# Kernel optimization log

Measured on AMD Instinct MI355X. Metric: run time of the kernel, lower is better.

Reference implementation:

```python
import jax, jax.numpy as jnp
import numpy as np

B, S, H = 1, 2048, 1024
NH, KVH, HD = 16, 4, 64
E, TOPK, F = 8, 2, 2048
EPS = 1e-5
THETA = 10000.0


def setup_inputs() -> dict:
    key = jax.random.key(0)
    ks = jax.random.split(key, 12)
    s = 0.02
    return {
        "hidden_states": jax.random.normal(ks[0], (B, S, H), jnp.float32),
        "position_ids": jnp.arange(S, dtype=jnp.int64).reshape(1, S),
        "ln1_w": jnp.ones((H,), jnp.float32),
        "ln2_w": jnp.ones((H,), jnp.float32),
        "wq": jax.random.normal(ks[1], (NH * HD, H), jnp.float32) * s,
        "wk": jax.random.normal(ks[2], (KVH * HD, H), jnp.float32) * s,
        "wv": jax.random.normal(ks[3], (KVH * HD, H), jnp.float32) * s,
        "wo": jax.random.normal(ks[4], (H, NH * HD), jnp.float32) * s,
        "gate_w": jax.random.normal(ks[5], (E, H), jnp.float32) * s,
        "w1": jax.random.normal(ks[6], (E, F, H), jnp.float32) * s,
        "w2": jax.random.normal(ks[7], (E, H, F), jnp.float32) * s,
        "w3": jax.random.normal(ks[8], (E, F, H), jnp.float32) * s,
    }


def rmsnorm(x, w, eps=EPS):
    xf = x.astype(jnp.float32)
    v = jnp.mean(xf * xf, axis=-1, keepdims=True)
    return (xf * jax.lax.rsqrt(v + eps)).astype(x.dtype) * w


def rotate_half(x):
    x1, x2 = jnp.split(x, 2, axis=-1)
    return jnp.concatenate([-x2, x1], axis=-1)


def attention(x, position_ids, wq, wk, wv, wo):
    q = (x @ wq.T).reshape(B, S, NH, HD).transpose(0, 2, 1, 3)   # [B,NH,S,HD]
    k = (x @ wk.T).reshape(B, S, KVH, HD).transpose(0, 2, 1, 3)  # [B,KVH,S,HD]
    v = (x @ wv.T).reshape(B, S, KVH, HD).transpose(0, 2, 1, 3)
    inv_freq = 1.0 / (THETA ** (jnp.arange(0, HD, 2, dtype=jnp.float32) / HD))
    ang = position_ids.astype(jnp.float32)[:, :, None] * inv_freq  # [B,S,HD/2]
    emb = jnp.concatenate([ang, ang], axis=-1)                     # [B,S,HD]
    cos = jnp.cos(emb)[:, None]                                    # [B,1,S,HD]
    sin = jnp.sin(emb)[:, None]
    q = q * cos + rotate_half(q) * sin
    k = k * cos + rotate_half(k) * sin
    rep = NH // KVH
    k = jnp.repeat(k, rep, axis=1)
    v = jnp.repeat(v, rep, axis=1)
    scores = jnp.einsum("bhqd,bhkd->bhqk", q, k) / np.sqrt(HD).astype(np.float32)
    causal = jnp.tril(jnp.ones((S, S), bool))
    scores = jnp.where(causal, scores, jnp.finfo(scores.dtype).min)
    attn = jax.nn.softmax(scores, axis=-1)
    ctx = jnp.einsum("bhqk,bhkd->bhqd", attn, v)
    ctx = ctx.transpose(0, 2, 1, 3).reshape(B, S, NH * HD)
    return ctx @ wo.T


def moe(x, gate_w, w1, w2, w3):
    xt = x.reshape(-1, H)                                  # [T,H]
    router_logits = xt @ gate_w.T                          # [T,E]
    probs = jax.nn.softmax(router_logits.astype(jnp.float32), axis=-1)
    topw, topi = jax.lax.top_k(probs, TOPK)                # [T,K]
    topw = topw / jnp.sum(topw, axis=-1, keepdims=True)
    topw = topw.astype(x.dtype)
    # combine weights per expert: [T,E]
    cw = jnp.sum(topw[..., None] * jax.nn.one_hot(topi, E, dtype=x.dtype), axis=1)
    h1 = jnp.einsum("th,efh->etf", xt, w1)
    h3 = jnp.einsum("th,efh->etf", xt, w3)
    g = jax.nn.silu(h1) * h3                               # [E,T,F]
    y = jnp.einsum("etf,ehf->eth", g, w2)                  # [E,T,H]
    out = jnp.einsum("eth,te->th", y, cw)
    return out.reshape(B, S, H), router_logits


def reference(hidden_states, position_ids, ln1_w, ln2_w, wq, wk, wv, wo,
              gate_w, w1, w2, w3):
    residual = hidden_states
    h = rmsnorm(hidden_states, ln1_w)
    h = attention(h, position_ids, wq, wk, wv, wo)
    h = residual + h
    residual = h
    h = rmsnorm(h, ln2_w)
    h, router_logits = moe(h, gate_w, w1, w2, w3)
    h = residual + h
    return h, router_logits
```

## Files before the change

### kernel.cpp

```cpp
#include <hip/hip_runtime.h>
#include <hip/hip_bf16.h>
#include <cstdint>

typedef unsigned short u16;
typedef __attribute__((ext_vector_type(8))) short bh8;
typedef __attribute__((ext_vector_type(4))) short sh4;
typedef __attribute__((ext_vector_type(4))) float fx4;

#define NTOK 2048
#define HDIM 1024
#define NE 8
#define FDIM 2048

__device__ __forceinline__ u16 f2bf(float f) {
    __hip_bfloat16 h = __float2bfloat16(f);
    return __builtin_bit_cast(u16, h);
}

__device__ __forceinline__ void gll16(const void* g, void* l) {
    __builtin_amdgcn_global_load_lds(
        (const __attribute__((address_space(1))) void*)g,
        (__attribute__((address_space(3))) void*)l, 16, 0, 0);
}

__global__ __launch_bounds__(256)
void convert_k(const float* __restrict__ S, u16* __restrict__ D, int n8) {
    int i = blockIdx.x * 256 + threadIdx.x;
    const int stride = gridDim.x * 256;
    for (; i < n8; i += stride) {
        const fx4 a = *(const fx4*)&S[(size_t)i * 8];
        const fx4 b = *(const fx4*)&S[(size_t)i * 8 + 4];
        bh8 o;
        #pragma unroll
        for (int j = 0; j < 4; ++j) {
            o[j]     = (short)f2bf(a[j]);
            o[j + 4] = (short)f2bf(b[j]);
        }
        *(bh8*)&D[(size_t)i * 8] = o;
    }
}

__global__ __launch_bounds__(256)
void rope_table_k(float* __restrict__ cosT, float* __restrict__ sinT) {
    int idx = blockIdx.x * 256 + threadIdx.x;
    int t = idx >> 5, i = idx & 31;
    float freq = powf(10000.0f, -(float)i * (1.0f / 32.0f));
    float ang = (float)t * freq;
    float s, c;
    sincosf(ang, &s, &c);
    cosT[idx] = c;
    sinT[idx] = s;
}

__global__ __launch_bounds__(256)
void rmsnorm_k(const float* __restrict__ X, const float* __restrict__ W, u16* __restrict__ O) {
    const int t = blockIdx.x;
    const int tid = threadIdx.x;
    const fx4 v = *(const fx4*)&X[(size_t)t * HDIM + tid * 4];
    float ss = v[0]*v[0] + v[1]*v[1] + v[2]*v[2] + v[3]*v[3];
    #pragma unroll
    for (int o = 1; o < 64; o <<= 1) ss += __shfl_xor(ss, o);
    __shared__ float red[4];
    if ((tid & 63) == 0) red[tid >> 6] = ss;
    __syncthreads();
    const float inv = rsqrtf((red[0] + red[1] + red[2] + red[3]) * (1.0f / HDIM) + 1e-5f);
// ... 22 lines not shown
    fx4 xn;
    #pragma unroll
    for (int i = 0; i < 4; ++i) xn[i] = v[i] * inv * w[i];
    sh4 o4;
    #pragma unroll
    for (int i = 0; i < 4; ++i) o4[i] = (short)f2bf(xn[i]);
    *(sh4*)&O[(size_t)t * HDIM + tid * 4] = o4;

    float part[NE];
    #pragma unroll
    for (int e = 0; e < NE; ++e) {
        const fx4 g = *(const fx4*)&GW[(size_t)e * HDIM + tid * 4];
        part[e] = g[0]*xn[0] + g[1]*xn[1] + g[2]*xn[2] + g[3]*xn[3];
    }
    #pragma unroll
    for (int e = 0; e < NE; ++e)
        #pragma unroll
        for (int o = 1; o < 64; o <<= 1) part[e] += __shfl_xor(part[e], o);
    __shared__ float red8[4][NE];
    if ((tid & 63) == 0) {
        #pragma unroll
        for (int e = 0; e < NE; ++e) red8[tid >> 6][e] = part[e];
    }
    __syncthreads();
    if (tid < NE)
        LOGI[(size_t)t * NE + tid] = red8[0][tid] + red8[1][tid] + red8[2][tid] + red8[3][tid];
}

__global__ __launch_bounds__(256)
void router_topk_k(const float* __restrict__ LOGI, int* __restrict__ counts,
                   int* __restrict__ tokslot, float* __restrict__ wtb) {
    const int t = blockIdx.x * 256 + threadIdx.x;
    float l[NE];
    #pragma unroll
    for (int e = 0; e < NE; ++e) l[e] = LOGI[(size_t)t * NE + e];
    int i0 = 0;
    #pragma unroll
    for (int e = 1; e < NE; ++e) if (l[e] > l[i0]) i0 = e;
    int i1 = (i0 == 0) ? 1 : 0;
    #pragma unroll
    for (int e = 0; e < NE; ++e) if (e != i0 && l[e] > l[i1]) i1 = e;
    float e1 = __expf(l[i1] - l[i0]);
    float w0 = 1.0f / (1.0f + e1);
    float w1 = 1.0f - w0;
    int p0 = atomicAdd(&counts[i0], 1);
    tokslot[i0 * NTOK + p0] = t * 2;
    wtb[i0 * NTOK + p0] = w0;
    int p1 = atomicAdd(&counts[i1], 1);
    tokslot[i1 * NTOK + p1] = t * 2 + 1;
    wtb[i1 * NTOK + p1] = w1;
}

template<int EPI>
__global__ __launch_bounds__(256)
void gemm_bt(const u16* __restrict__ A, const u16* __restrict__ B,
             u16* __restrict__ Cb, float* __restrict__ Cf,
             const int N, const int K,
             const float* __restrict__ aux0, const float* __restrict__ aux1) {
    __shared__ u16 As[2][64 * 32];
    __shared__ u16 Bs[2][64 * 32];

    const int tid = threadIdx.x;
    const int lane = tid & 63;
    const int wid = tid >> 6;
    const int lrow = lane & 15, lgrp = lane >> 4;
    const int wm = wid * 16;

    const int m0 = blockIdx.y * 64;
    const int n0 = blockIdx.x * 64;

    const u16* apg = A + (size_t)(m0 + (tid >> 2)) * K + (tid & 3) * 8;
    const u16* bpg = B + (size_t)(n0 + (tid >> 2)) * K + (tid & 3) * 8;

    fx4 acc[4];
    #pragma unroll
    for (int i = 0; i < 4; ++i) acc[i] = fx4{0.f, 0.f, 0.f, 0.f};

    gll16(apg, &As[0][wid * 512]);
    gll16(bpg, &Bs[0][wid * 512]);
    int cur = 0;
    for (int k0 = 0; k0 < K; k0 += 32) {
        __syncthreads();
        if (k0 + 32 < K) {
            gll16(apg + k0 + 32, &As[cur ^ 1][wid * 512]);
            gll16(bpg + k0 + 32, &Bs[cur ^ 1][wid * 512]);
        }
        const bh8 af = *(const bh8*)&As[cur][(wm + lrow) * 32 + lgrp * 8];
        #pragma unroll
        for (int ni = 0; ni < 4; ++ni) {
            const bh8 bf = *(const bh8*)&Bs[cur][(ni * 16 + lrow) * 32 + lgrp * 8];
            acc[ni] = __builtin_amdgcn_mfma_f32_16x16x32_bf16(af, bf, acc[ni], 0, 0, 0);
        }
        cur ^= 1;
    }

    #pragma unroll
    for (int j = 0; j < 4; ++j) {
        const int r = m0 + wm + lgrp * 4 + j;
        if (EPI == 3) {
            #pragma unroll
            for (int ni = 0; ni < 2; ++ni) {
                const int d = ni * 16 + lrow;
                const float cv = aux0[r * 32 + d];
                const float sv = aux1[r * 32 + d];
                const float v0 = acc[ni][j];
                const float v1 = acc[ni + 2][j];
                Cb[(size_t)r * N + n0 + d]      = f2bf(v0 * cv - v1 * sv);
                Cb[(size_t)r * N + n0 + d + 32] = f2bf(v1 * cv + v0 * sv);
            }
        } else {
            #pragma unroll
            for (int ni = 0; ni < 4; ++ni) {
                const int c = n0 + ni * 16 + lrow;
                const float v = acc[ni][j];
                if (EPI == 1) Cf[(size_t)r * N + c] = v + aux0[(size_t)r * N + c];
                if (EPI == 2) Cb[(size_t)r * N + c] = f2bf(v);
            }
        }
    }
}

__global__ __launch_bounds__(256)
void attn_kernel(const u16* __restrict__ Q, const u16* __restrict__ Kg,
                 const u16* __restrict__ Vg, u16* __restrict__ O) {
    const int qt = blockIdx.x;
    const int h = blockIdx.y;
    const int kvh = h >> 2;

    const int tid = threadIdx.x;
    const int lane = tid & 63;
    const int wid = tid >> 6;
    const int lrow = lane & 15, lgrp = lane >> 4;

    __shared__ u16 Ks[64 * 72];
    __shared__ u16 Vs[64 * 72];
    __shared__ u16 Ps[4][32 * 72];

    const int qbase = qt * 128 + wid * 32;

    bh8 qf[2][2];
    #pragma unroll
    for (int mi = 0; mi < 2; ++mi)
        #pragma unroll
        for (int kf = 0; kf < 2; ++kf)
            qf[mi][kf] = *(const bh8*)&Q[(size_t)(qbase + mi * 16 + lrow) * 1024 + h * 64 + kf * 32 + lgrp * 8];

    fx4 acc[2][4];
    #pragma unroll
    for (int mi = 0; mi < 2; ++mi)
        #pragma unroll
        for (int ni = 0; ni < 4; ++ni) acc[mi][ni] = fx4{0.f, 0.f, 0.f, 0.f};
    float mrun[2][4], lrun[2][4];
    #pragma unroll
    for (int mi = 0; mi < 2; ++mi)
        #pragma unroll
        for (int j = 0; j < 4; ++j) { mrun[mi][j] = -1e30f; lrun[mi][j] = 0.f; }

    const int srow = tid >> 2;
    const int sseg = (tid & 3) * 16;

    const int ntiles = qt * 2 + 2;

    size_t goff = (size_t)(srow) * 256 + kvh * 64 + sseg;
    bh8 kva = *(const bh8*)&Kg[goff];
    bh8 kvb = *(const bh8*)&Kg[goff + 8];
    bh8 vva = *(const bh8*)&Vg[goff];
    bh8 vvb = *(const bh8*)&Vg[goff + 8];

    for (int it = 0; it < ntiles; ++it) {
// ... 56 lines not shown
                const float alpha = __expf(mrun[mi][j] - mnew);
                mrun[mi][j] = mnew;
                float rsum = 0.f;
                #pragma unroll
                for (int nf = 0; nf < 4; ++nf) {
                    const float p = __expf(s[mi][nf][j] - mnew);
                    s[mi][nf][j] = p;
                    rsum += p;
                }
                #pragma unroll
                for (int o = 1; o < 16; o <<= 1) rsum += __shfl_xor(rsum, o);
                lrun[mi][j] = lrun[mi][j] * alpha + rsum;
                #pragma unroll
                for (int ni = 0; ni < 4; ++ni) acc[mi][ni][j] *= alpha;
            }

        u16* pw = Ps[wid];
        #pragma unroll
        for (int mi = 0; mi < 2; ++mi)
            #pragma unroll
            for (int nf = 0; nf < 4; ++nf)
                #pragma unroll
                for (int j = 0; j < 4; ++j)
                    pw[(mi * 16 + lgrp * 4 + j) * 72 + nf * 16 + lrow] = f2bf(s[mi][nf][j]);

        #pragma unroll
        for (int kf = 0; kf < 2; ++kf) {
            bh8 pa[2];
            #pragma unroll
            for (int mi = 0; mi < 2; ++mi)
                pa[mi] = *(const bh8*)&pw[(mi * 16 + lrow) * 72 + kf * 32 + lgrp * 8];
            #pragma unroll
            for (int ni = 0; ni < 4; ++ni) {
                bh8 vb = *(const bh8*)&Vs[(ni * 16 + lrow) * 72 + kf * 32 + lgrp * 8];
                #pragma unroll
                for (int mi = 0; mi < 2; ++mi)
                    acc[mi][ni] = __builtin_amdgcn_mfma_f32_16x16x32_bf16(pa[mi], vb, acc[mi][ni], 0, 0, 0);
            }
        }
    }

    #pragma unroll
    for (int mi = 0; mi < 2; ++mi)
        #pragma unroll
        for (int j = 0; j < 4; ++j) {
            const float inv = 1.0f / lrun[mi][j];
            const int r = qbase + mi * 16 + lgrp * 4 + j;
            #pragma unroll
            for (int ni = 0; ni < 4; ++ni)
                O[(size_t)r * 1024 + h * 64 + ni * 16 + lrow] = f2bf(acc[mi][ni][j] * inv);
        }
}

__global__ __launch_bounds__(256)
void moe_up_k(const u16* __restrict__ X, const u16* __restrict__ W1b,
              const u16* __restrict__ W3b, const int* __restrict__ counts,
              const int* __restrict__ tokslot, u16* __restrict__ G) {
    const int e = blockIdx.z;
    const int cnt = counts[e];
    const int m0 = blockIdx.y * 64;
    if (m0 >= cnt) return;
    const int n0 = blockIdx.x * 128;

    __shared__ u16 As[2][64 * 32];
    __shared__ u16 B1s[2][128 * 32];
    __shared__ u16 B3s[2][128 * 32];

    const int tid = threadIdx.x;
    const int lane = tid & 63, wid = tid >> 6;
    const int wm = (wid >> 1) * 32, wn = (wid & 1) * 64;
    const int lrow = lane & 15, lgrp = lane >> 4;

    const int p = m0 + (tid >> 2);
    const int tok = (p < cnt) ? (tokslot[e * NTOK + p] >> 1) : 0;
    const u16* apg  = X + (size_t)tok * HDIM + (tid & 3) * 8;
    const u16* b1pg = W1b + (size_t)e * FDIM * HDIM + (size_t)(n0 + (tid >> 2)) * HDIM + (tid & 3) * 8;
    const u16* b3pg = W3b + (size_t)e * FDIM * HDIM + (size_t)(n0 + (tid >> 2)) * HDIM + (tid & 3) * 8;

    fx4 acc1[2][4], acc3[2][4];
    #pragma unroll
    for (int i = 0; i < 2; ++i)
        #pragma unroll
        for (int j = 0; j < 4; ++j) {
            acc1[i][j] = fx4{0.f, 0.f, 0.f, 0.f};
            acc3[i][j] = fx4{0.f, 0.f, 0.f, 0.f};
        }

    gll16(apg, &As[0][wid * 512]);
    gll16(b1pg, &B1s[0][wid * 512]);
    gll16(b1pg + (size_t)64 * HDIM, &B1s[0][2048 + wid * 512]);
    gll16(b3pg, &B3s[0][wid * 512]);
    gll16(b3pg + (size_t)64 * HDIM, &B3s[0][2048 + wid * 512]);

    int cur = 0;
    for (int k0 = 0; k0 < HDIM; k0 += 32) {
        __syncthreads();
        if (k0 + 32 < HDIM) {
            const int kn = k0 + 32;
            gll16(apg + kn, &As[cur ^ 1][wid * 512]);
            gll16(b1pg + kn, &B1s[cur ^ 1][wid * 512]);
            gll16(b1pg + (size_t)64 * HDIM + kn, &B1s[cur ^ 1][2048 + wid * 512]);
            gll16(b3pg + kn, &B3s[cur ^ 1][wid * 512]);
            gll16(b3pg + (size_t)64 * HDIM + kn, &B3s[cur ^ 1][2048 + wid * 512]);
        }
        bh8 af[2];
        #pragma unroll
        for (int mi = 0; mi < 2; ++mi)
            af[mi] = *(const bh8*)&As[cur][(wm + mi * 16 + lrow) * 32 + lgrp * 8];
        #pragma unroll
        for (int ni = 0; ni < 4; ++ni) {
            const bh8 b1f = *(const bh8*)&B1s[cur][(wn + ni * 16 + lrow) * 32 + lgrp * 8];
            const bh8 b3f = *(const bh8*)&B3s[cur][(wn + ni * 16 + lrow) * 32 + lgrp * 8];
            #pragma unroll
            for (int mi = 0; mi < 2; ++mi) {
                acc1[mi][ni] = __builtin_amdgcn_mfma_f32_16x16x32_bf16(af[mi], b1f, acc1[mi][ni], 0, 0, 0);
                acc3[mi][ni] = __builtin_amdgcn_mfma_f32_16x16x32_bf16(af[mi], b3f, acc3[mi][ni], 0, 0, 0);
            }
        }
        cur ^= 1;
    }

    #pragma unroll
    for (int mi = 0; mi < 2; ++mi)
        #pragma unroll
        for (int j = 0; j < 4; ++j) {
            const int r = m0 + wm + mi * 16 + lgrp * 4 + j;
            if (r < cnt) {
                #pragma unroll
                for (int ni = 0; ni < 4; ++ni) {
                    const int c = n0 + wn + ni * 16 + lrow;
                    const float h1 = acc1[mi][ni][j];
                    const float h3 = acc3[mi][ni][j];
                    const float gv = h1 / (1.0f + __expf(-h1)) * h3;
                    G[((size_t)e * NTOK + r) * FDIM + c] = f2bf(gv);
                }
            }
        }
}

__global__ __launch_bounds__(256)
void moe_down_k(const u16* __restrict__ G, const u16* __restrict__ W2b,
                const int* __restrict__ counts, const int* __restrict__ tokslot,
                const float* __restrict__ wtb, float* __restrict__ MO) {
    const int e = blockIdx.z;
    const int cnt = counts[e];
    const int m0 = blockIdx.y * 64;
    if (m0 >= cnt) return;
    const int n0 = blockIdx.x * 64;

    __shared__ u16 As[2][64 * 32];
    __shared__ u16 Bs[2][64 * 32];

    const int tid = threadIdx.x;
    const int lane = tid & 63, wid = tid >> 6;
    const int wm = wid * 16;
    const int lrow = lane & 15, lgrp = lane >> 4;

    const u16* apg = G + ((size_t)e * NTOK + m0 + (tid >> 2)) * FDIM + (tid & 3) * 8;
    const u16* bpg = W2b + (size_t)e * HDIM * FDIM + (size_t)(n0 + (tid >> 2)) * FDIM + (tid & 3) * 8;

    fx4 acc[4];
    #pragma unroll
    for (int i = 0; i < 4; ++i) acc[i] = fx4{0.f, 0.f, 0.f, 0.f};

    gll16(apg, &As[0][wid * 512]);
    gll16(bpg, &Bs[0][wid * 512]);
    int cur = 0;
    for (int k0 = 0; k0 < FDIM; k0 += 32) {
        __syncthreads();
        if (k0 + 32 < FDIM) {
            gll16(apg + k0 + 32, &As[cur ^ 1][wid * 512]);
            gll16(bpg + k0 + 32, &Bs[cur ^ 1][wid * 512]);
        }
        const bh8 af = *(const bh8*)&As[cur][(wm + lrow) * 32 + lgrp * 8];
        #pragma unroll
        for (int ni = 0; ni < 4; ++ni) {
            const bh8 bf = *(const bh8*)&Bs[cur][(ni * 16 + lrow) * 32 + lgrp * 8];
            acc[ni] = __builtin_amdgcn_mfma_f32_16x16x32_bf16(af, bf, acc[ni], 0, 0, 0);
        }
        cur ^= 1;
    }

    #pragma unroll
    for (int j = 0; j < 4; ++j) {
        const int r = m0 + wm + lgrp * 4 + j;
        if (r < cnt) {
            const int ts = tokslot[e * NTOK + r];
            const float wgt = wtb[e * NTOK + r];
            const int tt = ts >> 1;
            const int sl = ts & 1;
            #pragma unroll
            for (int ni = 0; ni < 4; ++ni) {
                const int c = n0 + ni * 16 + lrow;
                MO[((size_t)sl * NTOK + tt) * HDIM + c] = acc[ni][j] * wgt;
            }
        }
    }
}

__global__ __launch_bounds__(256)
void final_add_k(const float* __restrict__ A, const float* __restrict__ B0,
                 const float* __restrict__ B1, float* __restrict__ O) {
    const size_t i = ((size_t)blockIdx.x * 256 + threadIdx.x) * 4;
    const fx4 a = *(const fx4*)&A[i];
    const fx4 b = *(const fx4*)&B0[i];
    const fx4 c = *(const fx4*)&B1[i];
    fx4 r;
    #pragma unroll
    for (int k = 0; k < 4; ++k) r[k] = a[k] + b[k] + c[k];
    *(fx4*)&O[i] = r;
}

extern "C" void kernel_launch(void* const* d_in, const int* in_sizes, int n_in,
                              void* d_out, int out_size, void* d_ws, size_t ws_size,
                              hipStream_t stream) {
    const float* x   = (const float*)d_in[0];
    const float* ln1 = (const float*)d_in[2];
    const float* ln2 = (const float*)d_in[3];
    const float* wq  = (const float*)d_in[4];
    const float* wk  = (const float*)d_in[5];
    const float* wv  = (const float*)d_in[6];
    const float* wo  = (const float*)d_in[7];
    const float* gw  = (const float*)d_in[8];
    const float* w1  = (const float*)d_in[9];
    const float* w2  = (const float*)d_in[10];
    const float* w3  = (const float*)d_in[11];

    float* out_h = (float*)d_out;
    float* out_logits = out_h + (size_t)NTOK * HDIM;

    uint8_t* wsb = (uint8_t*)d_ws;
    size_t off = 0;
    auto alloc = [&](size_t bytes) -> void* {
        void* ptr = wsb + off;
        off = (off + bytes + 255) & ~(size_t)255;
        return ptr;
    };
    u16*   xn1    = (u16*)alloc((size_t)NTOK * HDIM * 2);
    u16*   qb     = (u16*)alloc((size_t)NTOK * 1024 * 2);
    u16*   kb     = (u16*)alloc((size_t)NTOK * 256 * 2);
    u16*   vb     = (u16*)alloc((size_t)NTOK * 256 * 2);
    u16*   ctxb   = (u16*)alloc((size_t)NTOK * 1024 * 2);
    float* hattn  = (float*)alloc((size_t)NTOK * HDIM * 4);
    u16*   xn2    = (u16*)alloc((size_t)NTOK * HDIM * 2);
    float* cosT   = (float*)alloc((size_t)NTOK * 32 * 4);
    float* sinT   = (float*)alloc((size_t)NTOK * 32 * 4);
    int*   counts = (int*)alloc(NE * 4);
    int*   tokslot= (int*)alloc((size_t)NE * NTOK * 4);
    float* wtb    = (float*)alloc((size_t)NE * NTOK * 4);
    u16*   gbuf   = (u16*)alloc((size_t)NE * NTOK * FDIM * 2);
    float* moeb   = (float*)alloc((size_t)2 * NTOK * HDIM * 4);
    u16*   wqb    = (u16*)alloc((size_t)1024 * HDIM * 2);
    u16*   wkb    = (u16*)alloc((size_t)256 * HDIM * 2);
    u16*   wvb    = (u16*)alloc((size_t)256 * HDIM * 2);
    u16*   wob    = (u16*)alloc((size_t)HDIM * 1024 * 2);
    u16*   w1b    = (u16*)alloc((size_t)NE * FDIM * HDIM * 2);
    u16*   w2b    = (u16*)alloc((size_t)NE * HDIM * FDIM * 2);
    u16*   w3b    = (u16*)alloc((size_t)NE * FDIM * HDIM * 2);

    hipMemsetAsync(counts, 0, NE * 4, stream);

    convert_k<<<512, 256, 0, stream>>>(wq, wqb, 1024 * HDIM / 8);
    convert_k<<<128, 256, 0, stream>>>(wk, wkb, 256 * HDIM / 8);
    convert_k<<<128, 256, 0, stream>>>(wv, wvb, 256 * HDIM / 8);
    convert_k<<<512, 256, 0, stream>>>(wo, wob, HDIM * 1024 / 8);
    convert_k<<<2048, 256, 0, stream>>>(w1, w1b, NE * FDIM * HDIM / 8);
    convert_k<<<2048, 256, 0, stream>>>(w2, w2b, NE * HDIM * FDIM / 8);
    convert_k<<<2048, 256, 0, stream>>>(w3, w3b, NE * FDIM * HDIM / 8);

    rope_table_k<<<256, 256, 0, stream>>>(cosT, sinT);
    rmsnorm_k<<<NTOK, 256, 0, stream>>>(x, ln1, xn1);
    gemm_bt<3><<<dim3(16, 32), 256, 0, stream>>>(xn1, wqb, qb, nullptr, 1024, HDIM, cosT, sinT);
    gemm_bt<3><<<dim3(4, 32), 256, 0, stream>>>(xn1, wkb, kb, nullptr, 256, HDIM, cosT, sinT);
    gemm_bt<2><<<dim3(4, 32), 256, 0, stream>>>(xn1, wvb, vb, nullptr, 256, HDIM, nullptr, nullptr);
    attn_kernel<<<dim3(16, 16), 256, 0, stream>>>(qb, kb, vb, ctxb);
    gemm_bt<1><<<dim3(16, 32), 256, 0, stream>>>(ctxb, wob, nullptr, hattn, 1024, 1024, x, nullptr);
    rmsnorm2_router_k<<<NTOK, 256, 0, stream>>>(hattn, ln2, gw, xn2, out_logits);
    router_topk_k<<<8, 256, 0, stream>>>(out_logits, counts, tokslot, wtb);
    moe_up_k<<<dim3(16, 32, NE), 256, 0, stream>>>(xn2, w1b, w3b, counts, tokslot, gbuf);
    moe_down_k<<<dim3(16, 32, NE), 256, 0, stream>>>(gbuf, w2b, counts, tokslot, wtb, moeb);
    final_add_k<<<NTOK, 256, 0, stream>>>(hattn, moeb, moeb + (size_t)NTOK * HDIM, out_h);
}
```

Baseline: 408.2 us.

## Load A fragments directly to registers and swizzle B tiles in LDS

In the dense GEMM, MoE up and MoE down kernels, the A operand no longer goes through shared memory. Each lane loads its MFMA fragment straight from global memory into registers, prefetched one k-step ahead. The B tile gets an XOR swizzle on both the global-to-LDS write and the fragment read, to avoid LDS bank conflicts. The main loop is unrolled by two with explicit ping-pong buffers, halving the LDS footprint for A and removing its staging traffic, at the cost of uncoalesced per-lane global reads and extra registers.

After: 438.7 us. 1.07x slower.

```diff
diff --git a/kernel.cpp b/kernel.cpp
--- a/kernel.cpp
+++ b/kernel.cpp
@@ -144,7 +144,6 @@
              u16* __restrict__ Cb, float* __restrict__ Cf,
              const int N, const int K,
              const float* __restrict__ aux0, const float* __restrict__ aux1) {
-    __shared__ u16 As[2][64 * 32];
     __shared__ u16 Bs[2][64 * 32];
 
     const int tid = threadIdx.x;
@@ -152,33 +151,42 @@
     const int wid = tid >> 6;
     const int lrow = lane & 15, lgrp = lane >> 4;
     const int wm = wid * 16;
+    const int soff = (lgrp ^ ((lrow >> 1) & 3)) * 8;
 
     const int m0 = blockIdx.y * 64;
     const int n0 = blockIdx.x * 64;
 
-    const u16* apg = A + (size_t)(m0 + (tid >> 2)) * K + (tid & 3) * 8;
-    const u16* bpg = B + (size_t)(n0 + (tid >> 2)) * K + (tid & 3) * 8;
+    const int gseg = ((tid & 3) ^ ((tid >> 3) & 3)) * 8;
+    const u16* bpg = B + (size_t)(n0 + (tid >> 2)) * K + gseg;
+    const u16* apg = A + (size_t)(m0 + wm + lrow) * K + lgrp * 8;
 
     fx4 acc[4];
     #pragma unroll
     for (int i = 0; i < 4; ++i) acc[i] = fx4{0.f, 0.f, 0.f, 0.f};
 
-    gll16(apg, &As[0][wid * 512]);
     gll16(bpg, &Bs[0][wid * 512]);
-    int cur = 0;
-    for (int k0 = 0; k0 < K; k0 += 32) {
-        __syncthreads();
-        if (k0 + 32 < K) {
-            gll16(apg + k0 + 32, &As[cur ^ 1][wid * 512]);
-            gll16(bpg + k0 + 32, &Bs[cur ^ 1][wid * 512]);
-        }
-        const bh8 af = *(const bh8*)&As[cur][(wm + lrow) * 32 + lgrp * 8];
+    bh8 a0 = *(const bh8*)(apg);
+    bh8 a1;
+
+    for (int k0 = 0; k0 < K; k0 += 64) {
+        __syncthreads();
+        gll16(bpg + k0 + 32, &Bs[1][wid * 512]);
+        a1 = *(const bh8*)(apg + k0 + 32);
         #pragma unroll
         for (int ni = 0; ni < 4; ++ni) {
-            const bh8 bf = *(const bh8*)&Bs[cur][(ni * 16 + lrow) * 32 + lgrp * 8];
-            acc[ni] = __builtin_amdgcn_mfma_f32_16x16x32_bf16(af, bf, acc[ni], 0, 0, 0);
-        }
-        cur ^= 1;
+            const bh8 bf = *(const bh8*)&Bs[0][(ni * 16 + lrow) * 32 + soff];
+            acc[ni] = __builtin_amdgcn_mfma_f32_16x16x32_bf16(a0, bf, acc[ni], 0, 0, 0);
+        }
+        __syncthreads();
+        if (k0 + 64 < K) {
+            gll16(bpg + k0 + 64, &Bs[0][wid * 512]);
+            a0 = *(const bh8*)(apg + k0 + 64);
+        }
+        #pragma unroll
+        for (int ni = 0; ni < 4; ++ni) {
+            const bh8 bf = *(const bh8*)&Bs[1][(ni * 16 + lrow) * 32 + soff];
+            acc[ni] = __builtin_amdgcn_mfma_f32_16x16x32_bf16(a1, bf, acc[ni], 0, 0, 0);
+        }
     }
 
     #pragma unroll
@@ -374,7 +382,6 @@
     if (m0 >= cnt) return;
     const int n0 = blockIdx.x * 128;
 
-    __shared__ u16 As[2][64 * 32];
     __shared__ u16 B1s[2][128 * 32];
     __shared__ u16 B3s[2][128 * 32];
 
@@ -382,12 +389,20 @@
     const int lane = tid & 63, wid = tid >> 6;
     const int wm = (wid >> 1) * 32, wn = (wid & 1) * 64;
     const int lrow = lane & 15, lgrp = lane >> 4;
-
-    const int p = m0 + (tid >> 2);
-    const int tok = (p < cnt) ? (tokslot[e * NTOK + p] >> 1) : 0;
-    const u16* apg  = X + (size_t)tok * HDIM + (tid & 3) * 8;
-    const u16* b1pg = W1b + (size_t)e * FDIM * HDIM + (size_t)(n0 + (tid >> 2)) * HDIM + (tid & 3) * 8;
-    const u16* b3pg = W3b + (size_t)e * FDIM * HDIM + (size_t)(n0 + (tid >> 2)) * HDIM + (tid & 3) * 8;
+    const int soff = (lgrp ^ ((lrow >> 1) & 3)) * 8;
+
+    const int r0i = m0 + wm + lrow;
+    const int r1i = r0i + 16;
+    const int tk0 = (r0i < cnt) ? (tokslot[e * NTOK + r0i] >> 1) : 0;
+    const int tk1 = (r1i < cnt) ? (tokslot[e * NTOK + r1i] >> 1) : 0;
+    const u16* ap0 = X + (size_t)tk0 * HDIM + lgrp * 8;
+    const u16* ap1 = X + (size_t)tk1 * HDIM + lgrp * 8;
+
+    const int gseg = ((tid & 3) ^ ((tid >> 3) & 3)) * 8;
+    const size_t eoff = (size_t)e * FDIM * HDIM;
+    const u16* b1pg = W1b + eoff + (size_t)(n0 + (tid >> 2)) * HDIM + gseg;
+    const u16* b3pg = W3b + eoff + (size_t)(n0 + (tid >> 2)) * HDIM + gseg;
+    const size_t sw2 = (size_t)64 * HDIM;
 
     fx4 acc1[2][4], acc3[2][4];
     #pragma unroll
@@ -398,38 +413,55 @@
             acc3[i][j] = fx4{0.f, 0.f, 0.f, 0.f};
         }
 
-    gll16(apg, &As[0][wid * 512]);
     gll16(b1pg, &B1s[0][wid * 512]);
-    gll16(b1pg + (size_t)64 * HDIM, &B1s[0][2048 + wid * 512]);
+    gll16(b1pg + sw2, &B1s[0][2048 + wid * 512]);
     gll16(b3pg, &B3s[0][wid * 512]);
-    gll16(b3pg + (size_t)64 * HDIM, &B3s[0][2048 + wid * 512]);
-
-    int cur = 0;
-    for (int k0 = 0; k0 < HDIM; k0 += 32) {
-        __syncthreads();
-        if (k0 + 32 < HDIM) {
+    gll16(b3pg + sw2, &B3s[0][2048 + wid * 512]);
+    bh8 a00 = *(const bh8*)(ap0);
+    bh8 a01 = *(const bh8*)(ap1);
+    bh8 a10, a11;
+
+    for (int k0 = 0; k0 < HDIM; k0 += 64) {
+        __syncthreads();
+        {
             const int kn = k0 + 32;
-            gll16(apg + kn, &As[cur ^ 1][wid * 512]);
-            gll16(b1pg + kn, &B1s[cur ^ 1][wid * 512]);
-            gll16(b1pg + (size_t)64 * HDIM + kn, &B1s[cur ^ 1][2048 + wid * 512]);
-            gll16(b3pg + kn, &B3s[cur ^ 1][wid * 512]);
-            gll16(b3pg + (size_t)64 * HDIM + kn, &B3s[cur ^ 1][2048 + wid * 512]);
-        }
-        bh8 af[2];
-        #pragma unroll
-        for (int mi = 0; mi < 2; ++mi)
-            af[mi] = *(const bh8*)&As[cur][(wm + mi * 16 + lrow) * 32 + lgrp * 8];
+            gll16(b1pg + kn, &B1s[1][wid * 512]);
+            gll16(b1pg + sw2 + kn, &B1s[1][2048 + wid * 512]);
+            gll16(b3pg + kn, &B3s[1][wid * 512]);
+            gll16(b3pg + sw2 + kn, &B3s[1][2048 + wid * 512]);
+            a10 = *(const bh8*)(ap0 + kn);
+            a11 = *(const bh8*)(ap1 + kn);
+        }
         #pragma unroll
         for (int ni = 0; ni < 4; ++ni) {
-            const bh8 b1f = *(const bh8*)&B1s[cur][(wn + ni * 16 + lrow) * 32 + lgrp * 8];
-            const bh8 b3f = *(const bh8*)&B3s[cur][(wn + ni * 16 + lrow) * 32 + lgrp * 8];
-            #pragma unroll
-            for (int mi = 0; mi < 2; ++mi) {
-                acc1[mi][ni] = __builtin_amdgcn_mfma_f32_16x16x32_bf16(af[mi], b1f, acc1[mi][ni], 0, 0, 0);
-                acc3[mi][ni] = __builtin_amdgcn_mfma_f32_16x16x32_bf16(af[mi], b3f, acc3[mi][ni], 0, 0, 0);
-            }
-        }
-        cur ^= 1;
+            const int ro = (wn + ni * 16 + lrow) * 32 + soff;
+            const bh8 b1f = *(const bh8*)&B1s[0][ro];
+            const bh8 b3f = *(const bh8*)&B3s[0][ro];
+            acc1[0][ni] = __builtin_amdgcn_mfma_f32_16x16x32_bf16(a00, b1f, acc1[0][ni], 0, 0, 0);
+            acc3[0][ni] = __builtin_amdgcn_mfma_f32_16x16x32_bf16(a00, b3f, acc3[0][ni], 0, 0, 0);
+            acc1[1][ni] = __builtin_amdgcn_mfma_f32_16x16x32_bf16(a01, b1f, acc1[1][ni], 0, 0, 0);
+            acc3[1][ni] = __builtin_amdgcn_mfma_f32_16x16x32_bf16(a01, b3f, acc3[1][ni], 0, 0, 0);
+        }
+        __syncthreads();
+        if (k0 + 64 < HDIM) {
+            const int kn = k0 + 64;
+            gll16(b1pg + kn, &B1s[0][wid * 512]);
+            gll16(b1pg + sw2 + kn, &B1s[0][2048 + wid * 512]);
+            gll16(b3pg + kn, &B3s[0][wid * 512]);
+            gll16(b3pg + sw2 + kn, &B3s[0][2048 + wid * 512]);
+            a00 = *(const bh8*)(ap0 + kn);
+            a01 = *(const bh8*)(ap1 + kn);
+        }
+        #pragma unroll
+        for (int ni = 0; ni < 4; ++ni) {
+            const int ro = (wn + ni * 16 + lrow) * 32 + soff;
+            const bh8 b1f = *(const bh8*)&B1s[1][ro];
+            const bh8 b3f = *(const bh8*)&B3s[1][ro];
+            acc1[0][ni] = __builtin_amdgcn_mfma_f32_16x16x32_bf16(a10, b1f, acc1[0][ni], 0, 0, 0);
+            acc3[0][ni] = __builtin_amdgcn_mfma_f32_16x16x32_bf16(a10, b3f, acc3[0][ni], 0, 0, 0);
+            acc1[1][ni] = __builtin_amdgcn_mfma_f32_16x16x32_bf16(a11, b1f, acc1[1][ni], 0, 0, 0);
+            acc3[1][ni] = __builtin_amdgcn_mfma_f32_16x16x32_bf16(a11, b3f, acc3[1][ni], 0, 0, 0);
+        }
     }
 
     #pragma unroll
@@ -460,37 +492,45 @@
     if (m0 >= cnt) return;
     const int n0 = blockIdx.x * 64;
 
-    __shared__ u16 As[2][64 * 32];
     __shared__ u16 Bs[2][64 * 32];
 
     const int tid = threadIdx.x;
     const int lane = tid & 63, wid = tid >> 6;
     const int wm = wid * 16;
     const int lrow = lane & 15, lgrp = lane >> 4;
-
-    const u16* apg = G + ((size_t)e * NTOK + m0 + (tid >> 2)) * FDIM + (tid & 3) * 8;
-    const u16* bpg = W2b + (size_t)e * HDIM * FDIM + (size_t)(n0 + (tid >> 2)) * FDIM + (tid & 3) * 8;
+    const int soff = (lgrp ^ ((lrow >> 1) & 3)) * 8;
+
+    const int gseg = ((tid & 3) ^ ((tid >> 3) & 3)) * 8;
+    const u16* bpg = W2b + (size_t)e * HDIM * FDIM + (size_t)(n0 + (tid >> 2)) * FDIM + gseg;
+    const u16* apg = G + ((size_t)e * NTOK + m0 + wm + lrow) * FDIM + lgrp * 8;
 
     fx4 acc[4];
     #pragma unroll
     for (int i = 0; i < 4; ++i) acc[i] = fx4{0.f, 0.f, 0.f, 0.f};
 
-    gll16(apg, &As[0][wid * 512]);
     gll16(bpg, &Bs[0][wid * 512]);
-    int cur = 0;
-    for (int k0 = 0; k0 < FDIM; k0 += 32) {
-        __syncthreads();
-        if (k0 + 32 < FDIM) {
-            gll16(apg + k0 + 32, &As[cur ^ 1][wid * 512]);
-            gll16(bpg + k0 + 32, &Bs[cur ^ 1][wid * 512]);
-        }
-        const bh8 af = *(const bh8*)&As[cur][(wm + lrow) * 32 + lgrp * 8];
+    bh8 a0 = *(const bh8*)(apg);
+    bh8 a1;
+
+    for (int k0 = 0; k0 < FDIM; k0 += 64) {
+        __syncthreads();
+        gll16(bpg + k0 + 32, &Bs[1][wid * 512]);
+        a1 = *(const bh8*)(apg + k0 + 32);
         #pragma unroll
         for (int ni = 0; ni < 4; ++ni) {
-            const bh8 bf = *(const bh8*)&Bs[cur][(ni * 16 + lrow) * 32 + lgrp * 8];
-            acc[ni] = __builtin_amdgcn_mfma_f32_16x16x32_bf16(af, bf, acc[ni], 0, 0, 0);
-        }
-        cur ^= 1;
+            const bh8 bf = *(const bh8*)&Bs[0][(ni * 16 + lrow) * 32 + soff];
+            acc[ni] = __builtin_amdgcn_mfma_f32_16x16x32_bf16(a0, bf, acc[ni], 0, 0, 0);
+        }
+        __syncthreads();
+        if (k0 + 64 < FDIM) {
+            gll16(bpg + k0 + 64, &Bs[0][wid * 512]);
+            a0 = *(const bh8*)(apg + k0 + 64);
+        }
+        #pragma unroll
+        for (int ni = 0; ni < 4; ++ni) {
+            const bh8 bf = *(const bh8*)&Bs[1][(ni * 16 + lrow) * 32 + soff];
+            acc[ni] = __builtin_amdgcn_mfma_f32_16x16x32_bf16(a1, bf, acc[ni], 0, 0, 0);
+        }
     }
 
     #pragma unroll
```

## Rewrite GEMMs as single-wave blocks with swizzled LDS and explicit waitcnt pipelining

Applied to the files above, without the earlier changes.

Converts the dense, MoE up and MoE down GEMM kernels from 4-wave 256-thread blocks to single-wave 64-thread blocks with 32x64 tiles. Each wave now computes a 2x4 MFMA tile from double-buffered LDS filled by direct global-to-LDS loads. Explicit vmcnt/lgkmcnt waits and sched barriers replace __syncthreads, and an XOR swizzle is meant to avoid LDS bank conflicts. This removes block-wide barriers and raises the number of blocks, at the cost of smaller tiles per block and more global traffic for the weight operand. It also relies on the single wave seeing its own direct-to-LDS writes without a barrier.

Result: no change. 411.0 us (+0.7%).

```diff
diff --git a/kernel.cpp b/kernel.cpp
--- a/kernel.cpp
+++ b/kernel.cpp
@@ -11,6 +11,10 @@
 #define HDIM 1024
 #define NE 8
 #define FDIM 2048
+
+#define VMCNT(n) asm volatile("s_waitcnt vmcnt(" #n ")" ::: "memory")
+#define LGKM0()  asm volatile("s_waitcnt lgkmcnt(0)" ::: "memory")
+#define SCB()    __builtin_amdgcn_sched_barrier(0)
 
 __device__ __forceinline__ u16 f2bf(float f) {
     __hip_bfloat16 h = __float2bfloat16(f);
@@ -139,69 +143,99 @@
 }
 
 template<int EPI>
-__global__ __launch_bounds__(256)
+__global__ __launch_bounds__(64)
 void gemm_bt(const u16* __restrict__ A, const u16* __restrict__ B,
              u16* __restrict__ Cb, float* __restrict__ Cf,
              const int N, const int K,
              const float* __restrict__ aux0, const float* __restrict__ aux1) {
-    __shared__ u16 As[2][64 * 32];
+    __shared__ u16 As[2][32 * 32];
     __shared__ u16 Bs[2][64 * 32];
 
-    const int tid = threadIdx.x;
-    const int lane = tid & 63;
-    const int wid = tid >> 6;
-    const int lrow = lane & 15, lgrp = lane >> 4;
-    const int wm = wid * 16;
-
-    const int m0 = blockIdx.y * 64;
+    const int l = threadIdx.x;
+    const int lrow = l & 15, lgrp = l >> 4;
+    const int soff = (lgrp ^ ((lrow >> 1) & 3)) * 8;
+
+    const int m0 = blockIdx.y * 32;
     const int n0 = blockIdx.x * 64;
 
-    const u16* apg = A + (size_t)(m0 + (tid >> 2)) * K + (tid & 3) * 8;
-    const u16* bpg = B + (size_t)(n0 + (tid >> 2)) * K + (tid & 3) * 8;
-
-    fx4 acc[4];
-    #pragma unroll
-    for (int i = 0; i < 4; ++i) acc[i] = fx4{0.f, 0.f, 0.f, 0.f};
-
-    gll16(apg, &As[0][wid * 512]);
-    gll16(bpg, &Bs[0][wid * 512]);
-    int cur = 0;
-    for (int k0 = 0; k0 < K; k0 += 32) {
-        __syncthreads();
-        if (k0 + 32 < K) {
-            gll16(apg + k0 + 32, &As[cur ^ 1][wid * 512]);
-            gll16(bpg + k0 + 32, &Bs[cur ^ 1][wid * 512]);
-        }
-        const bh8 af = *(const bh8*)&As[cur][(wm + lrow) * 32 + lgrp * 8];
-        #pragma unroll
-        for (int ni = 0; ni < 4; ++ni) {
-            const bh8 bf = *(const bh8*)&Bs[cur][(ni * 16 + lrow) * 32 + lgrp * 8];
-            acc[ni] = __builtin_amdgcn_mfma_f32_16x16x32_bf16(af, bf, acc[ni], 0, 0, 0);
-        }
-        cur ^= 1;
-    }
-
-    #pragma unroll
-    for (int j = 0; j < 4; ++j) {
-        const int r = m0 + wm + lgrp * 4 + j;
-        if (EPI == 3) {
-            #pragma unroll
-            for (int ni = 0; ni < 2; ++ni) {
-                const int d = ni * 16 + lrow;
-                const float cv = aux0[r * 32 + d];
-                const float sv = aux1[r * 32 + d];
-                const float v0 = acc[ni][j];
-                const float v1 = acc[ni + 2][j];
-                Cb[(size_t)r * N + n0 + d]      = f2bf(v0 * cv - v1 * sv);
-                Cb[(size_t)r * N + n0 + d + 32] = f2bf(v1 * cv + v0 * sv);
-            }
-        } else {
-            #pragma unroll
-            for (int ni = 0; ni < 4; ++ni) {
-                const int c = n0 + ni * 16 + lrow;
-                const float v = acc[ni][j];
-                if (EPI == 1) Cf[(size_t)r * N + c] = v + aux0[(size_t)r * N + c];
-                if (EPI == 2) Cb[(size_t)r * N + c] = f2bf(v);
+    const int srow = l >> 2;
+    const int sseg = ((l & 3) ^ ((l >> 3) & 3)) * 8;
+    const u16* ag = A + (size_t)(m0 + srow) * K + sseg;
+    const u16* bg = B + (size_t)(n0 + srow) * K + sseg;
+    const size_t r16a = (size_t)16 * K;
+
+    fx4 acc[2][4];
+    #pragma unroll
+    for (int i = 0; i < 2; ++i)
+        #pragma unroll
+        for (int j = 0; j < 4; ++j) acc[i][j] = fx4{0.f, 0.f, 0.f, 0.f};
+
+#define G_STAGE(BUF, KK)                                   \
+    gll16(ag + (KK), &As[BUF][0]);                         \
+    gll16(ag + r16a + (KK), &As[BUF][512]);                \
+    gll16(bg + (KK), &Bs[BUF][0]);                         \
+    gll16(bg + r16a + (KK), &Bs[BUF][512]);                \
+    gll16(bg + 2 * r16a + (KK), &Bs[BUF][1024]);           \
+    gll16(bg + 3 * r16a + (KK), &Bs[BUF][1536]);
+
+#define G_COMPUTE(BUF)                                                         \
+    {                                                                          \
+        bh8 af[2], bf[4];                                                      \
+        _Pragma("unroll")                                                      \
+        for (int mi = 0; mi < 2; ++mi)                                         \
+            af[mi] = *(const bh8*)&As[BUF][(mi * 16 + lrow) * 32 + soff];      \
+        _Pragma("unroll")                                                      \
+        for (int ni = 0; ni < 4; ++ni)                                         \
+            bf[ni] = *(const bh8*)&Bs[BUF][(ni * 16 + lrow) * 32 + soff];      \
+        _Pragma("unroll")                                                      \
+        for (int mi = 0; mi < 2; ++mi)                                         \
+            _Pragma("unroll")                                                  \
+            for (int ni = 0; ni < 4; ++ni)                                     \
+                acc[mi][ni] = __builtin_amdgcn_mfma_f32_16x16x32_bf16(af[mi], bf[ni], acc[mi][ni], 0, 0, 0); \
+    }
+
+    G_STAGE(0, 0)
+    for (int k0 = 0; k0 < K; k0 += 64) {
+        G_STAGE(1, k0 + 32)
+        VMCNT(6); SCB();
+        G_COMPUTE(0)
+        LGKM0(); SCB();
+        {
+            const int kn = (k0 + 64 < K) ? k0 + 64 : k0;
+            G_STAGE(0, kn)
+        }
+        VMCNT(6); SCB();
+        G_COMPUTE(1)
+        LGKM0(); SCB();
+    }
+    VMCNT(0);
+#undef G_STAGE
+#undef G_COMPUTE
+
+    #pragma unroll
+    for (int mi = 0; mi < 2; ++mi) {
+        #pragma unroll
+        for (int j = 0; j < 4; ++j) {
+            const int r = m0 + mi * 16 + lgrp * 4 + j;
+            if (EPI == 3) {
+                #pragma unroll
+                for (int ni = 0; ni < 2; ++ni) {
+                    const int d = ni * 16 + lrow;
+                    const float cv = aux0[r * 32 + d];
+                    const float sv = aux1[r * 32 + d];
+                    const float v0 = acc[mi][ni][j];
+                    const float v1 = acc[mi][ni + 2][j];
+                    Cb[(size_t)r * N + n0 + d]      = f2bf(v0 * cv - v1 * sv);
+                    Cb[(size_t)r * N + n0 + d + 32] = f2bf(v1 * cv + v0 * sv);
+                }
+            } else {
+                #pragma unroll
+                for (int ni = 0; ni < 4; ++ni) {
+                    const int c = n0 + ni * 16 + lrow;
+                    const float v = acc[mi][ni][j];
+                    if (EPI == 1) Cf[(size_t)r * N + c] = v + aux0[(size_t)r * N + c];
+                    if (EPI == 2) Cb[(size_t)r * N + c] = f2bf(v);
+                }
             }
         }
     }
@@ -364,30 +398,37 @@
         }
 }
 
-__global__ __launch_bounds__(256)
+__global__ __launch_bounds__(64)
 void moe_up_k(const u16* __restrict__ X, const u16* __restrict__ W1b,
               const u16* __restrict__ W3b, const int* __restrict__ counts,
               const int* __restrict__ tokslot, u16* __restrict__ G) {
     const int e = blockIdx.z;
     const int cnt = counts[e];
-    const int m0 = blockIdx.y * 64;
+    const int m0 = blockIdx.y * 32;
     if (m0 >= cnt) return;
-    const int n0 = blockIdx.x * 128;
-
-    __shared__ u16 As[2][64 * 32];
-    __shared__ u16 B1s[2][128 * 32];
-    __shared__ u16 B3s[2][128 * 32];
-
-    const int tid = threadIdx.x;
-    const int lane = tid & 63, wid = tid >> 6;
-    const int wm = (wid >> 1) * 32, wn = (wid & 1) * 64;
-    const int lrow = lane & 15, lgrp = lane >> 4;
-
-    const int p = m0 + (tid >> 2);
-    const int tok = (p < cnt) ? (tokslot[e * NTOK + p] >> 1) : 0;
-    const u16* apg  = X + (size_t)tok * HDIM + (tid & 3) * 8;
-    const u16* b1pg = W1b + (size_t)e * FDIM * HDIM + (size_t)(n0 + (tid >> 2)) * HDIM + (tid & 3) * 8;
-    const u16* b3pg = W3b + (size_t)e * FDIM * HDIM + (size_t)(n0 + (tid >> 2)) * HDIM + (tid & 3) * 8;
+    const int n0 = blockIdx.x * 64;
+
+    __shared__ u16 As[2][32 * 32];
+    __shared__ u16 B1s[2][64 * 32];
+    __shared__ u16 B3s[2][64 * 32];
+
+    const int l = threadIdx.x;
+    const int lrow = l & 15, lgrp = l >> 4;
+    const int soff = (lgrp ^ ((lrow >> 1) & 3)) * 8;
+
+    const int srow = l >> 2;
+    const int sseg = ((l & 3) ^ ((l >> 3) & 3)) * 8;
+    const int p0 = m0 + srow;
+    const int p1 = p0 + 16;
+    const int tk0 = (p0 < cnt) ? (tokslot[e * NTOK + p0] >> 1) : 0;
+    const int tk1 = (p1 < cnt) ? (tokslot[e * NTOK + p1] >> 1) : 0;
+    const u16* a0g = X + (size_t)tk0 * HDIM + sseg;
+    const u16* a1g = X + (size_t)tk1 * HDIM + sseg;
+
+    const size_t eoff = (size_t)e * FDIM * HDIM;
+    const u16* bg1 = W1b + eoff + (size_t)(n0 + srow) * HDIM + sseg;
+    const u16* bg3 = W3b + eoff + (size_t)(n0 + srow) * HDIM + sseg;
+    const size_t r16 = (size_t)16 * HDIM;
 
     fx4 acc1[2][4], acc3[2][4];
     #pragma unroll
@@ -398,49 +439,65 @@
             acc3[i][j] = fx4{0.f, 0.f, 0.f, 0.f};
         }
 
-    gll16(apg, &As[0][wid * 512]);
-    gll16(b1pg, &B1s[0][wid * 512]);
-    gll16(b1pg + (size_t)64 * HDIM, &B1s[0][2048 + wid * 512]);
-    gll16(b3pg, &B3s[0][wid * 512]);
-    gll16(b3pg + (size_t)64 * HDIM, &B3s[0][2048 + wid * 512]);
-
-    int cur = 0;
-    for (int k0 = 0; k0 < HDIM; k0 += 32) {
-        __syncthreads();
-        if (k0 + 32 < HDIM) {
-            const int kn = k0 + 32;
-            gll16(apg + kn, &As[cur ^ 1][wid * 512]);
-            gll16(b1pg + kn, &B1s[cur ^ 1][wid * 512]);
-            gll16(b1pg + (size_t)64 * HDIM + kn, &B1s[cur ^ 1][2048 + wid * 512]);
-            gll16(b3pg + kn, &B3s[cur ^ 1][wid * 512]);
-            gll16(b3pg + (size_t)64 * HDIM + kn, &B3s[cur ^ 1][2048 + wid * 512]);
-        }
-        bh8 af[2];
-        #pragma unroll
-        for (int mi = 0; mi < 2; ++mi)
-            af[mi] = *(const bh8*)&As[cur][(wm + mi * 16 + lrow) * 32 + lgrp * 8];
-        #pragma unroll
-        for (int ni = 0; ni < 4; ++ni) {
-            const bh8 b1f = *(const bh8*)&B1s[cur][(wn + ni * 16 + lrow) * 32 + lgrp * 8];
-            const bh8 b3f = *(const bh8*)&B3s[cur][(wn + ni * 16 + lrow) * 32 + lgrp * 8];
-            #pragma unroll
-            for (int mi = 0; mi < 2; ++mi) {
-                acc1[mi][ni] = __builtin_amdgcn_mfma_f32_16x16x32_bf16(af[mi], b1f, acc1[mi][ni], 0, 0, 0);
-                acc3[mi][ni] = __builtin_amdgcn_mfma_f32_16x16x32_bf16(af[mi], b3f, acc3[mi][ni], 0, 0, 0);
-            }
-        }
-        cur ^= 1;
-    }
+#define U_STAGE(BUF, KK)                                   \
+    gll16(a0g + (KK), &As[BUF][0]);                        \
+    gll16(a1g + (KK), &As[BUF][512]);                      \
+    gll16(bg1 + (KK), &B1s[BUF][0]);                       \
+    gll16(bg1 + r16 + (KK), &B1s[BUF][512]);               \
+    gll16(bg1 + 2 * r16 + (KK), &B1s[BUF][1024]);          \
+    gll16(bg1 + 3 * r16 + (KK), &B1s[BUF][1536]);          \
+    gll16(bg3 + (KK), &B3s[BUF][0]);                       \
+    gll16(bg3 + r16 + (KK), &B3s[BUF][512]);               \
+    gll16(bg3 + 2 * r16 + (KK), &B3s[BUF][1024]);          \
+    gll16(bg3 + 3 * r16 + (KK), &B3s[BUF][1536]);
+
+#define U_COMPUTE(BUF)                                                          \
+    {                                                                           \
+        bh8 af[2], b1f[4], b3f[4];                                              \
+        _Pragma("unroll")                                                       \
+        for (int mi = 0; mi < 2; ++mi)                                          \
+            af[mi] = *(const bh8*)&As[BUF][(mi * 16 + lrow) * 32 + soff];       \
+        _Pragma("unroll")                                                       \
+        for (int ni = 0; ni < 4; ++ni) {                                        \
+            b1f[ni] = *(const bh8*)&B1s[BUF][(ni * 16 + lrow) * 32 + soff];     \
+            b3f[ni] = *(const bh8*)&B3s[BUF][(ni * 16 + lrow) * 32 + soff];     \
+        }                                                                       \
+        _Pragma("unroll")                                                       \
+        for (int mi = 0; mi < 2; ++mi)                                          \
+            _Pragma("unroll")                                                   \
+            for (int ni = 0; ni < 4; ++ni) {                                    \
+                acc1[mi][ni] = __builtin_amdgcn_mfma_f32_16x16x32_bf16(af[mi], b1f[ni], acc1[mi][ni], 0, 0, 0); \
+                acc3[mi][ni] = __builtin_amdgcn_mfma_f32_16x16x32_bf16(af[mi], b3f[ni], acc3[mi][ni], 0, 0, 0); \
+            }                                                                   \
+    }
+
+    U_STAGE(0, 0)
+    for (int k0 = 0; k0 < HDIM; k0 += 64) {
+        U_STAGE(1, k0 + 32)
+        VMCNT(10); SCB();
+        U_COMPUTE(0)
+        LGKM0(); SCB();
+        {
+            const int kn = (k0 + 64 < HDIM) ? k0 + 64 : k0;
+            U_STAGE(0, kn)
+        }
+        VMCNT(10); SCB();
+        U_COMPUTE(1)
+        LGKM0(); SCB();
+    }
+    VMCNT(0);
+#undef U_STAGE
+#undef U_COMPUTE
 
     #pragma unroll
     for (int mi = 0; mi < 2; ++mi)
         #pragma unroll
         for (int j = 0; j < 4; ++j) {
-            const int r = m0 + wm + mi * 16 + lgrp * 4 + j;
+            const int r = m0 + mi * 16 + lgrp * 4 + j;
             if (r < cnt) {
                 #pragma unroll
                 for (int ni = 0; ni < 4; ++ni) {
-                    const int c = n0 + wn + ni * 16 + lrow;
+                    const int c = n0 + ni * 16 + lrow;
                     const float h1 = acc1[mi][ni][j];
                     const float h3 = acc3[mi][ni][j];
                     const float gv = h1 / (1.0f + __expf(-h1)) * h3;
@@ -450,64 +507,94 @@
         }
 }
 
-__global__ __launch_bounds__(256)
+__global__ __launch_bounds__(64)
 void moe_down_k(const u16* __restrict__ G, const u16* __restrict__ W2b,
                 const int* __restrict__ counts, const int* __restrict__ tokslot,
                 const float* __restrict__ wtb, float* __restrict__ MO) {
     const int e = blockIdx.z;
     const int cnt = counts[e];
-    const int m0 = blockIdx.y * 64;
+    const int m0 = blockIdx.y * 32;
     if (m0 >= cnt) return;
     const int n0 = blockIdx.x * 64;
 
-    __shared__ u16 As[2][64 * 32];
+    __shared__ u16 As[2][32 * 32];
     __shared__ u16 Bs[2][64 * 32];
 
-    const int tid = threadIdx.x;
-    const int lane = tid & 63, wid = tid >> 6;
-    const int wm = wid * 16;
-    const int lrow = lane & 15, lgrp = lane >> 4;
-
-    const u16* apg = G + ((size_t)e * NTOK + m0 + (tid >> 2)) * FDIM + (tid & 3) * 8;
-    const u16* bpg = W2b + (size_t)e * HDIM * FDIM + (size_t)(n0 + (tid >> 2)) * FDIM + (tid & 3) * 8;
-
-    fx4 acc[4];
-    #pragma unroll
-    for (int i = 0; i < 4; ++i) acc[i] = fx4{0.f, 0.f, 0.f, 0.f};
-
-    gll16(apg, &As[0][wid * 512]);
-    gll16(bpg, &Bs[0][wid * 512]);
-    int cur = 0;
-    for (int k0 = 0; k0 < FDIM; k0 += 32) {
-        __syncthreads();
-        if (k0 + 32 < FDIM) {
-            gll16(apg + k0 + 32, &As[cur ^ 1][wid * 512]);
-            gll16(bpg + k0 + 32, &Bs[cur ^ 1][wid * 512]);
-        }
-        const bh8 af = *(const bh8*)&As[cur][(wm + lrow) * 32 + lgrp * 8];
-        #pragma unroll
-        for (int ni = 0; ni < 4; ++ni) {
-            const bh8 bf = *(const bh8*)&Bs[cur][(ni * 16 + lrow) * 32 + lgrp * 8];
-            acc[ni] = __builtin_amdgcn_mfma_f32_16x16x32_bf16(af, bf, acc[ni], 0, 0, 0);
-        }
-        cur ^= 1;
-    }
-
-    #pragma unroll
-    for (int j = 0; j < 4; ++j) {
-        const int r = m0 + wm + lgrp * 4 + j;
-        if (r < cnt) {
-            const int ts = tokslot[e * NTOK + r];
-            const float wgt = wtb[e * NTOK + r];
-            const int tt = ts >> 1;
-            const int sl = ts & 1;
-            #pragma unroll
-            for (int ni = 0; ni < 4; ++ni) {
-                const int c = n0 + ni * 16 + lrow;
-                MO[((size_t)sl * NTOK + tt) * HDIM + c] = acc[ni][j] * wgt;
+    const int l = threadIdx.x;
+    const int lrow = l & 15, lgrp = l >> 4;
+    const int soff = (lgrp ^ ((lrow >> 1) & 3)) * 8;
+
+    const int srow = l >> 2;
+    const int sseg = ((l & 3) ^ ((l >> 3) & 3)) * 8;
+    const u16* ag = G + ((size_t)e * NTOK + m0 + srow) * FDIM + sseg;
+    const u16* bg = W2b + (size_t)e * HDIM * FDIM + (size_t)(n0 + srow) * FDIM + sseg;
+    const size_t r16 = (size_t)16 * FDIM;
+
+    fx4 acc[2][4];
+    #pragma unroll
+    for (int i = 0; i < 2; ++i)
+        #pragma unroll
+        for (int j = 0; j < 4; ++j) acc[i][j] = fx4{0.f, 0.f, 0.f, 0.f};
+
+#define D_STAGE(BUF, KK)                                   \
+    gll16(ag + (KK), &As[BUF][0]);                         \
+    gll16(ag + r16 + (KK), &As[BUF][512]);                 \
+    gll16(bg + (KK), &Bs[BUF][0]);                         \
+    gll16(bg + r16 + (KK), &Bs[BUF][512]);                 \
+    gll16(bg + 2 * r16 + (KK), &Bs[BUF][1024]);            \
+    gll16(bg + 3 * r16 + (KK), &Bs[BUF][1536]);
+
+#define D_COMPUTE(BUF)                                                         \
+    {                                                                          \
+        bh8 af[2], bf[4];                                                      \
+        _Pragma("unroll")                                                      \
+        for (int mi = 0; mi < 2; ++mi)                                         \
+            af[mi] = *(const bh8*)&As[BUF][(mi * 16 + lrow) * 32 + soff];      \
+        _Pragma("unroll")                                                      \
+        for (int ni = 0; ni < 4; ++ni)                                         \
+            bf[ni] = *(const bh8*)&Bs[BUF][(ni * 16 + lrow) * 32 + soff];      \
+        _Pragma("unroll")                                                      \
+        for (int mi = 0; mi < 2; ++mi)                                         \
+            _Pragma("unroll")                                                  \
+            for (int ni = 0; ni < 4; ++ni)                                     \
+                acc[mi][ni] = __builtin_amdgcn_mfma_f32_16x16x32_bf16(af[mi], bf[ni], acc[mi][ni], 0, 0, 0); \
+    }
+
+    D_STAGE(0, 0)
+    for (int k0 = 0; k0 < FDIM; k0 += 64) {
+        D_STAGE(1, k0 + 32)
+        VMCNT(6); SCB();
+        D_COMPUTE(0)
+        LGKM0(); SCB();
+        {
+            const int kn = (k0 + 64 < FDIM) ? k0 + 64 : k0;
+            D_STAGE(0, kn)
+        }
+        VMCNT(6); SCB();
+        D_COMPUTE(1)
+        LGKM0(); SCB();
+    }
+    VMCNT(0);
+#undef D_STAGE
+#undef D_COMPUTE
+
+    #pragma unroll
+    for (int mi = 0; mi < 2; ++mi)
+        #pragma unroll
+        for (int j = 0; j < 4; ++j) {
+            const int r = m0 + mi * 16 + lgrp * 4 + j;
+            if (r < cnt) {
+                const int ts = tokslot[e * NTOK + r];
+                const float wgt = wtb[e * NTOK + r];
+                const int tt = ts >> 1;
+                const int sl = ts & 1;
+                #pragma unroll
+                for (int ni = 0; ni < 4; ++ni) {
+                    const int c = n0 + ni * 16 + lrow;
+                    MO[((size_t)sl * NTOK + tt) * HDIM + c] = acc[mi][ni][j] * wgt;
+                }
             }
         }
-    }
 }
 
 __global__ __launch_bounds__(256)
@@ -582,14 +669,14 @@
 
     rope_table_k<<<256, 256, 0, stream>>>(cosT, sinT);
     rmsnorm_k<<<NTOK, 256, 0, stream>>>(x, ln1, xn1);
-    gemm_bt<3><<<dim3(16, 32), 256, 0, stream>>>(xn1, wqb, qb, nullptr, 1024, HDIM, cosT, sinT);
-    gemm_bt<3><<<dim3(4, 32), 256, 0, stream>>>(xn1, wkb, kb, nullptr, 256, HDIM, cosT, sinT);
-    gemm_bt<2><<<dim3(4, 32), 256, 0, stream>>>(xn1, wvb, vb, nullptr, 256, HDIM, nullptr, nullptr);
+    gemm_bt<3><<<dim3(16, 64), 64, 0, stream>>>(xn1, wqb, qb, nullptr, 1024, HDIM, cosT, sinT);
+    gemm_bt<3><<<dim3(4, 64), 64, 0, stream>>>(xn1, wkb, kb, nullptr, 256, HDIM, cosT, sinT);
+    gemm_bt<2><<<dim3(4, 64), 64, 0, stream>>>(xn1, wvb, vb, nullptr, 256, HDIM, nullptr, nullptr);
     attn_kernel<<<dim3(16, 16), 256, 0, stream>>>(qb, kb, vb, ctxb);
-    gemm_bt<1><<<dim3(16, 32), 256, 0, stream>>>(ctxb, wob, nullptr, hattn, 1024, 1024, x, nullptr);
+    gemm_bt<1><<<dim3(16, 64), 64, 0, stream>>>(ctxb, wob, nullptr, hattn, 1024, 1024, x, nullptr);
     rmsnorm2_router_k<<<NTOK, 256, 0, stream>>>(hattn, ln2, gw, xn2, out_logits);
     router_topk_k<<<8, 256, 0, stream>>>(out_logits, counts, tokslot, wtb);
-    moe_up_k<<<dim3(16, 32, NE), 256, 0, stream>>>(xn2, w1b, w3b, counts, tokslot, gbuf);
-    moe_down_k<<<dim3(16, 32, NE), 256, 0, stream>>>(gbuf, w2b, counts, tokslot, wtb, moeb);
+    moe_up_k<<<dim3(32, 64, NE), 64, 0, stream>>>(xn2, w1b, w3b, counts, tokslot, gbuf);
+    moe_down_k<<<dim3(16, 64, NE), 64, 0, stream>>>(gbuf, w2b, counts, tokslot, wtb, moeb);
     final_add_k<<<NTOK, 256, 0, stream>>>(hattn, moeb, moeb + (size_t)NTOK * HDIM, out_h);
 }
```
